# Optimization experiments

Measured on AMD Instinct MI355X. Metric: run time of the kernel, lower is better.

The kernel has to match this reference:

```python
import jax, jax.numpy as jnp
import numpy as np

CPV = 64  # cpv_size; output_size = CPV*(CPV+1)//2 = 2080

def _tri_indices(cpv):
    # Reproduce the torch nested-loop scatter order:
    # for idx_x in range(cpv): for idx_y in range(cpv-idx_x): col = cpv-1-idx_y
    rows = np.repeat(np.arange(cpv), cpv - np.arange(cpv))
    cols = np.concatenate([np.arange(cpv - 1, i - 1, -1) for i in range(cpv)])
    return jnp.asarray(rows), jnp.asarray(cols)


def setup_inputs() -> dict:
    key = jax.random.key(0)
    ks = jax.random.split(key, 12)
    B, D_in, H, L = 8192, 1024, 2048, CPV * (CPV + 1) // 2
    s = lambda fan_in: 1.0 / np.sqrt(fan_in)
    return {
        "x":   jax.random.normal(ks[0], (B, D_in), jnp.float32),
        "W1":  jax.random.uniform(ks[1], (D_in, H), jnp.float32, -s(D_in), s(D_in)),
        "b1":  jnp.zeros((H,), jnp.float32),
        "W2":  jax.random.uniform(ks[2], (H, H), jnp.float32, -s(H), s(H)),
        "b2":  jnp.zeros((H,), jnp.float32),
        "W21": jax.random.uniform(ks[3], (H, H), jnp.float32, -s(H), s(H)),
        "b21": jnp.zeros((H,), jnp.float32),
        "W22": jax.random.uniform(ks[4], (H, H), jnp.float32, -s(H), s(H)),
        "b22": jnp.zeros((H,), jnp.float32),
        "W3":  jax.random.uniform(ks[5], (H, L), jnp.float32, -s(H), s(H)),
        "b3":  jnp.zeros((L,), jnp.float32),
    }


def reference(x, W1, b1, W2, b2, W21, b21, W22, b22, W3, b3):
    lrelu = lambda t: jax.nn.leaky_relu(t, 0.01)
    h = lrelu(x @ W1 + b1)
    h = lrelu(h @ W2 + b2)
    h = lrelu(h @ W21 + b21)
    h = lrelu(h @ W22 + b22)
    y = h @ W3 + b3  # [B, L] with L = CPV*(CPV+1)//2
    rows, cols = _tri_indices(CPV)
    is_diag = rows == cols  # diagonal entries are abs'ed (negated when <= 0)
    vals = jnp.where(is_diag[None, :] & (y <= 0), -y, y)
    B = y.shape[0]
    M = jnp.zeros((B, CPV, CPV), y.dtype).at[:, rows, cols].set(vals)
    return jnp.transpose(M, (1, 2, 0))  # torch stacks per-example matrices on dim=2
```

## Files before the change

kernel.cpp:

```cpp
#include <hip/hip_runtime.h>
#include <hip/hip_bf16.h>
#include <stdint.h>

typedef short short8 __attribute__((ext_vector_type(8)));
typedef float f32x4  __attribute__((ext_vector_type(4)));

typedef __attribute__((address_space(1))) uint32_t u32_g;
typedef __attribute__((address_space(3))) uint32_t u32_l;

#define BM 128
#define BN 128
#define BK 64

__device__ __forceinline__ void gld_lds16(const void* g, const void* l) {
  __builtin_amdgcn_global_load_lds((u32_g*)(uintptr_t)g, (u32_l*)(uintptr_t)l, 16, 0, 0);
}

template <int FINAL>
__global__ __launch_bounds__(256) void gemm_k(
    const __hip_bfloat16* __restrict__ A,
    const __hip_bfloat16* __restrict__ BT,
    const float* __restrict__ bias,
    __hip_bfloat16* __restrict__ Cb,
    float* __restrict__ Cf,
    const int* __restrict__ tbl,
    int K, int Nreal)
{
  __shared__ __attribute__((aligned(16))) __hip_bfloat16 As[BM * BK];
  __shared__ __attribute__((aligned(16))) __hip_bfloat16 Bs[BN * BK];

  const int tid  = threadIdx.x;
  const int lane = tid & 63;
  const int l15  = lane & 15;
  const int quad = lane >> 4;
  const int wave = tid >> 6;
  const int wm   = (wave >> 1) << 6;
  const int wn   = (wave & 1) << 6;

  const int bm = blockIdx.x * BM;
  const int bn = blockIdx.y * BN;

  const __hip_bfloat16* ag[4];
  const __hip_bfloat16* bg[4];
  uint32_t lofs[4];
#pragma unroll
  for (int c = 0; c < 4; ++c) {
    int ci   = tid + 256 * c;
    int row  = ci >> 3;
    int chk  = ci & 7;
    int gchk = chk ^ (row & 7);
    ag[c]   = A  + (size_t)(bm + row) * K + gchk * 8;
    bg[c]   = BT + (size_t)(bn + row) * K + gchk * 8;
    lofs[c] = (uint32_t)ci * 16u;
  }

  f32x4 acc[4][4];
#pragma unroll
  for (int i = 0; i < 4; ++i)
#pragma unroll
    for (int j = 0; j < 4; ++j)
      acc[i][j] = (f32x4){0.f, 0.f, 0.f, 0.f};

  const int nk = K >> 6;
  for (int kt = 0; kt < nk; ++kt) {
#pragma unroll
    for (int c = 0; c < 4; ++c) {
      gld_lds16(ag[c], (const char*)As + lofs[c]);
      gld_lds16(bg[c], (const char*)Bs + lofs[c]);
      ag[c] += BK;
      bg[c] += BK;
    }
    __syncthreads();
#pragma unroll
    for (int ks = 0; ks < 2; ++ks) {
      short8 af[4], bf[4];
      const int cf = ks * 4 + quad;
#pragma unroll
      for (int i = 0; i < 4; ++i) {
        int m  = wm + i * 16 + l15;
        int sc = cf ^ (m & 7);
        af[i]  = *(const short8*)(As + m * BK + sc * 8);
      }
#pragma unroll
      for (int j = 0; j < 4; ++j) {
        int n  = wn + j * 16 + l15;
        int sc = cf ^ (n & 7);
        bf[j]  = *(const short8*)(Bs + n * BK + sc * 8);
      }
#pragma unroll
      for (int i = 0; i < 4; ++i)
#pragma unroll
        for (int j = 0; j < 4; ++j)
          acc[i][j] = __builtin_amdgcn_mfma_f32_16x16x32_bf16(af[i], bf[j], acc[i][j], 0, 0, 0);
    }
    __syncthreads();
  }

  if (FINAL == 0) {
#pragma unroll
    for (int j = 0; j < 4; ++j) {
      int   n  = bn + wn + j * 16 + l15;
      float bv = bias[n];
#pragma unroll
      for (int i = 0; i < 4; ++i) {
        int m0 = bm + wm + i * 16 + quad * 4;
#pragma unroll
        for (int r = 0; r < 4; ++r) {
          float v = acc[i][j][r] + bv;
          v = (v > 0.f) ? v : 0.01f * v;
          Cb[(size_t)(m0 + r) * 2048 + n] = __float2bfloat16(v);
        }
      }
    }
  } else {
#pragma unroll
    for (int j = 0; j < 4; ++j) {
      int n = bn + wn + j * 16 + l15;
      if (n < Nreal) {
        float bv   = bias[n];
        int  code  = tbl[n];
        int  dst   = code & 4095;
        bool diag  = (code & 4096) != 0;
#pragma unroll
        for (int i = 0; i < 4; ++i) {
          int m0 = bm + wm + i * 16 + quad * 4;
          f32x4 pk;
#pragma unroll
          for (int r = 0; r < 4; ++r) {
            float v = acc[i][j][r] + bv;
            if (diag) v = fabsf(v);
            pk[r] = v;
          }
          *reinterpret_cast<f32x4*>(Cf + (size_t)dst * 8192 + m0) = pk;
        }
      }
    }
  }
}

__global__ void transpose_k(const float* __restrict__ in,
                            __hip_bfloat16* __restrict__ out,
                            int K, int N)
{
  __shared__ __hip_bfloat16 t[32][33];
  const int n0 = blockIdx.x * 32;
  const int k0 = blockIdx.y * 32;
  const int tx = threadIdx.x, ty = threadIdx.y;
  const __hip_bfloat16 zero = __float2bfloat16(0.f);
#pragma unroll
  for (int r = 0; r < 32; r += 8) {
    int k = k0 + ty + r, n = n0 + tx;
    t[ty + r][tx] = (n < N) ? __float2bfloat16(in[(size_t)k * N + n]) : zero;
  }
  __syncthreads();
#pragma unroll
  for (int r = 0; r < 32; r += 8) {
    int n = n0 + ty + r;
    out[(size_t)n * K + k0 + tx] = t[tx][ty + r];
  }
}

__global__ void cvt_k(const float* __restrict__ in,
                      __hip_bfloat16* __restrict__ out, int n)
{
  int i = (blockIdx.x * 256 + threadIdx.x) * 4;
  if (i >= n) return;
  float4 v = *reinterpret_cast<const float4*>(in + i);
  union { unsigned short us[4]; uint2 v2; } pk;
  __hip_bfloat16 h;
  h = __float2bfloat16(v.x); pk.us[0] = *reinterpret_cast<unsigned short*>(&h);
  h = __float2bfloat16(v.y); pk.us[1] = *reinterpret_cast<unsigned short*>(&h);
  h = __float2bfloat16(v.z); pk.us[2] = *reinterpret_cast<unsigned short*>(&h);
  h = __float2bfloat16(v.w); pk.us[3] = *reinterpret_cast<unsigned short*>(&h);
  *reinterpret_cast<uint2*>(out + i) = pk.v2;
}

__global__ void table_k(int* __restrict__ tbl)
{
  int l = blockIdx.x * 64 + threadIdx.x;
  if (l >= 2080) return;
  int r = 0, s = 0;
  while (s + (64 - r) <= l) { s += 64 - r; ++r; }
  int c = 63 - (l - s);
  tbl[l] = (r * 64 + c) | ((r == c) ? 4096 : 0);
}

extern "C" void kernel_launch(void* const* d_in, const int* in_sizes, int n_in,
                              void* d_out, int out_size, void* d_ws, size_t ws_size,
                              hipStream_t stream)
{
  const float* x   = (const float*)d_in[0];
  const float* W1  = (const float*)d_in[1];
  const float* b1  = (const float*)d_in[2];
  const float* W2  = (const float*)d_in[3];
  const float* b2  = (const float*)d_in[4];
  const float* W21 = (const float*)d_in[5];
  const float* b21 = (const float*)d_in[6];
  const float* W22 = (const float*)d_in[7];
  const float* b22 = (const float*)d_in[8];
  const float* W3  = (const float*)d_in[9];
  const float* b3  = (const float*)d_in[10];
  float* out = (float*)d_out;

  char* ws = (char*)d_ws;
  __hip_bfloat16* act0 = (__hip_bfloat16*)(ws);
  __hip_bfloat16* act1 = (__hip_bfloat16*)(ws + ((size_t)32 << 20));
  __hip_bfloat16* xb   = act1;
  __hip_bfloat16* W1T  = (__hip_bfloat16*)(ws + ((size_t)64 << 20));
  __hip_bfloat16* W2T  = (__hip_bfloat16*)(ws + ((size_t)68 << 20));
  __hip_bfloat16* W21T = (__hip_bfloat16*)(ws + ((size_t)76 << 20));
  __hip_bfloat16* W22T = (__hip_bfloat16*)(ws + ((size_t)84 << 20));
  __hip_bfloat16* W3T  = (__hip_bfloat16*)(ws + ((size_t)92 << 20));
  int*            tbl  = (int*)(ws + ((size_t)101 << 20));

  hipMemsetAsync(d_out, 0, (size_t)out_size * sizeof(float), stream);
  table_k<<<33, 64, 0, stream>>>(tbl);

  cvt_k<<<8192, 256, 0, stream>>>(x, xb, 8192 * 1024);

  dim3 tb(32, 8);
  transpose_k<<<dim3(64, 32), tb, 0, stream>>>(W1,  W1T,  1024, 2048);
  transpose_k<<<dim3(64, 64), tb, 0, stream>>>(W2,  W2T,  2048, 2048);
  transpose_k<<<dim3(64, 64), tb, 0, stream>>>(W21, W21T, 2048, 2048);
  transpose_k<<<dim3(64, 64), tb, 0, stream>>>(W22, W22T, 2048, 2048);
  transpose_k<<<dim3(68, 64), tb, 0, stream>>>(W3,  W3T,  2048, 2080);

  gemm_k<0><<<dim3(64, 16), 256, 0, stream>>>(xb,   W1T,  b1,  act0, nullptr, nullptr, 1024, 2048);
  gemm_k<0><<<dim3(64, 16), 256, 0, stream>>>(act0, W2T,  b2,  act1, nullptr, nullptr, 2048, 2048);
  gemm_k<0><<<dim3(64, 16), 256, 0, stream>>>(act1, W21T, b21, act0, nullptr, nullptr, 2048, 2048);
  gemm_k<0><<<dim3(64, 16), 256, 0, stream>>>(act0, W22T, b22, act1, nullptr, nullptr, 2048, 2048);
  gemm_k<1><<<dim3(64, 17), 256, 0, stream>>>(act1, W3T,  b3,  nullptr, out,  tbl,     2048, 2080);
}
```

Before: 615.3 us.

## Use 256x256 tiles with triple-buffered async LDS pipeline and fused zero fill

```diff
diff --git a/kernel.cpp b/kernel.cpp
--- a/kernel.cpp
+++ b/kernel.cpp
@@ -8,16 +8,18 @@
 typedef __attribute__((address_space(1))) uint32_t u32_g;
 typedef __attribute__((address_space(3))) uint32_t u32_l;
 
-#define BM 128
-#define BN 128
-#define BK 64
+#define BM 256
+#define BN 256
+#define BK 32
+#define SLOTB 32768
+#define BOFF  16384
 
 __device__ __forceinline__ void gld_lds16(const void* g, const void* l) {
   __builtin_amdgcn_global_load_lds((u32_g*)(uintptr_t)g, (u32_l*)(uintptr_t)l, 16, 0, 0);
 }
 
 template <int FINAL>
-__global__ __launch_bounds__(256) void gemm_k(
+__global__ __launch_bounds__(512, 2) void gemm_k(
     const __hip_bfloat16* __restrict__ A,
     const __hip_bfloat16* __restrict__ BT,
     const float* __restrict__ bias,
@@ -26,74 +28,105 @@
     const int* __restrict__ tbl,
     int K, int Nreal)
 {
-  __shared__ __attribute__((aligned(16))) __hip_bfloat16 As[BM * BK];
-  __shared__ __attribute__((aligned(16))) __hip_bfloat16 Bs[BN * BK];
+  __shared__ __attribute__((aligned(16))) char smem[3 * SLOTB];
 
   const int tid  = threadIdx.x;
   const int lane = tid & 63;
   const int l15  = lane & 15;
   const int quad = lane >> 4;
   const int wave = tid >> 6;
-  const int wm   = (wave >> 1) << 6;
-  const int wn   = (wave & 1) << 6;
+  const int wm   = (wave >> 2) * 128;
+  const int wn   = (wave & 3) * 64;
 
   const int bm = blockIdx.x * BM;
   const int bn = blockIdx.y * BN;
 
-  const __hip_bfloat16* ag[4];
-  const __hip_bfloat16* bg[4];
-  uint32_t lofs[4];
-#pragma unroll
-  for (int c = 0; c < 4; ++c) {
-    int ci   = tid + 256 * c;
-    int row  = ci >> 3;
-    int chk  = ci & 7;
-    int gchk = chk ^ (row & 7);
-    ag[c]   = A  + (size_t)(bm + row) * K + gchk * 8;
-    bg[c]   = BT + (size_t)(bn + row) * K + gchk * 8;
-    lofs[c] = (uint32_t)ci * 16u;
-  }
-
-  f32x4 acc[4][4];
-#pragma unroll
-  for (int i = 0; i < 4; ++i)
+  const int arow = wm + l15;
+  const uint32_t aoff = (uint32_t)arow * 64u + (uint32_t)(((quad + (arow >> 1)) & 3) << 4);
+  const int brow = wn + l15;
+  const uint32_t boff = BOFF + (uint32_t)brow * 64u + (uint32_t)(((quad + (brow >> 1)) & 3) << 4);
+
+  const __hip_bfloat16* ag[2];
+  const __hip_bfloat16* bg[2];
+  uint32_t dA[2], dB[2];
+#pragma unroll
+  for (int c = 0; c < 2; ++c) {
+    int ci  = tid + 512 * c;
+    int row = ci >> 2;
+    int gc  = ((ci & 3) - (row >> 1)) & 3;
+    ag[c] = A  + (size_t)(bm + row) * K + gc * 8;
+    bg[c] = BT + (size_t)(bn + row) * K + gc * 8;
+    dA[c] = (uint32_t)ci * 16u;
+    dB[c] = BOFF + (uint32_t)ci * 16u;
+  }
+
+  f32x4 acc[8][4];
+#pragma unroll
+  for (int i = 0; i < 8; ++i)
 #pragma unroll
     for (int j = 0; j < 4; ++j)
       acc[i][j] = (f32x4){0.f, 0.f, 0.f, 0.f};
 
-  const int nk = K >> 6;
-  for (int kt = 0; kt < nk; ++kt) {
-#pragma unroll
-    for (int c = 0; c < 4; ++c) {
-      gld_lds16(ag[c], (const char*)As + lofs[c]);
-      gld_lds16(bg[c], (const char*)Bs + lofs[c]);
+  const int nk = K >> 5;
+
+#pragma unroll
+  for (int t = 0; t < 2; ++t) {
+    char* stb = smem + t * SLOTB;
+#pragma unroll
+    for (int c = 0; c < 2; ++c) {
+      gld_lds16(ag[c], stb + dA[c]);
+      gld_lds16(bg[c], stb + dB[c]);
       ag[c] += BK;
       bg[c] += BK;
     }
-    __syncthreads();
-#pragma unroll
-    for (int ks = 0; ks < 2; ++ks) {
-      short8 af[4], bf[4];
-      const int cf = ks * 4 + quad;
-#pragma unroll
-      for (int i = 0; i < 4; ++i) {
-        int m  = wm + i * 16 + l15;
-        int sc = cf ^ (m & 7);
-        af[i]  = *(const short8*)(As + m * BK + sc * 8);
+  }
+
+  int cur = 0, nst = 2;
+  for (int kt = 0; kt < nk; ++kt) {
+    if (kt < nk - 1) asm volatile("s_waitcnt vmcnt(4) lgkmcnt(0)" ::: "memory");
+    else             asm volatile("s_waitcnt vmcnt(0) lgkmcnt(0)" ::: "memory");
+    __builtin_amdgcn_s_barrier();
+    asm volatile("" ::: "memory");
+
+    const char* rb  = smem + cur * SLOTB;
+    char*       stb = smem + nst * SLOTB;
+
+    if (kt < nk - 2) {
+#pragma unroll
+      for (int c = 0; c < 2; ++c) {
+        gld_lds16(ag[c], stb + dA[c]);
+        gld_lds16(bg[c], stb + dB[c]);
+        ag[c] += BK;
+        bg[c] += BK;
       }
-#pragma unroll
-      for (int j = 0; j < 4; ++j) {
-        int n  = wn + j * 16 + l15;
-        int sc = cf ^ (n & 7);
-        bf[j]  = *(const short8*)(Bs + n * BK + sc * 8);
-      }
-#pragma unroll
-      for (int i = 0; i < 4; ++i)
-#pragma unroll
-        for (int j = 0; j < 4; ++j)
-          acc[i][j] = __builtin_amdgcn_mfma_f32_16x16x32_bf16(af[i], bf[j], acc[i][j], 0, 0, 0);
-    }
-    __syncthreads();
+    }
+
+    short8 bf[4], af[4];
+#pragma unroll
+    for (int j = 0; j < 4; ++j) bf[j] = *(const short8*)(rb + boff + j * 1024);
+#pragma unroll
+    for (int i = 0; i < 4; ++i) af[i] = *(const short8*)(rb + aoff + i * 1024);
+    __builtin_amdgcn_s_setprio(1);
+#pragma unroll
+    for (int i = 0; i < 4; ++i)
+#pragma unroll
+      for (int j = 0; j < 4; ++j)
+        acc[i][j] = __builtin_amdgcn_mfma_f32_16x16x32_bf16(af[i], bf[j], acc[i][j], 0, 0, 0);
+    __builtin_amdgcn_s_setprio(0);
+
+    short8 af2[4];
+#pragma unroll
+    for (int i = 0; i < 4; ++i) af2[i] = *(const short8*)(rb + aoff + 4096 + i * 1024);
+    __builtin_amdgcn_s_setprio(1);
+#pragma unroll
+    for (int i = 0; i < 4; ++i)
+#pragma unroll
+      for (int j = 0; j < 4; ++j)
+        acc[i + 4][j] = __builtin_amdgcn_mfma_f32_16x16x32_bf16(af2[i], bf[j], acc[i + 4][j], 0, 0, 0);
+    __builtin_amdgcn_s_setprio(0);
+
+    cur = (cur == 2) ? 0 : cur + 1;
+    nst = (nst == 2) ? 0 : nst + 1;
   }
 
   if (FINAL == 0) {
@@ -102,7 +135,7 @@
       int   n  = bn + wn + j * 16 + l15;
       float bv = bias[n];
 #pragma unroll
-      for (int i = 0; i < 4; ++i) {
+      for (int i = 0; i < 8; ++i) {
         int m0 = bm + wm + i * 16 + quad * 4;
 #pragma unroll
         for (int r = 0; r < 4; ++r) {
@@ -121,8 +154,10 @@
         int  code  = tbl[n];
         int  dst   = code & 4095;
         bool diag  = (code & 4096) != 0;
-#pragma unroll
-        for (int i = 0; i < 4; ++i) {
+        int  mir   = ((dst & 63) << 6) | (dst >> 6);
+        const f32x4 z = (f32x4){0.f, 0.f, 0.f, 0.f};
+#pragma unroll
+        for (int i = 0; i < 8; ++i) {
           int m0 = bm + wm + i * 16 + quad * 4;
           f32x4 pk;
 #pragma unroll
@@ -132,6 +167,8 @@
             pk[r] = v;
           }
           *reinterpret_cast<f32x4*>(Cf + (size_t)dst * 8192 + m0) = pk;
+          if (!diag)
+            *reinterpret_cast<f32x4*>(Cf + (size_t)mir * 8192 + m0) = z;
         }
       }
     }
@@ -213,7 +250,6 @@
   __hip_bfloat16* W3T  = (__hip_bfloat16*)(ws + ((size_t)92 << 20));
   int*            tbl  = (int*)(ws + ((size_t)101 << 20));
 
-  hipMemsetAsync(d_out, 0, (size_t)out_size * sizeof(float), stream);
   table_k<<<33, 64, 0, stream>>>(tbl);
 
   cvt_k<<<8192, 256, 0, stream>>>(x, xb, 8192 * 1024);
@@ -223,11 +259,11 @@
   transpose_k<<<dim3(64, 64), tb, 0, stream>>>(W2,  W2T,  2048, 2048);
   transpose_k<<<dim3(64, 64), tb, 0, stream>>>(W21, W21T, 2048, 2048);
   transpose_k<<<dim3(64, 64), tb, 0, stream>>>(W22, W22T, 2048, 2048);
-  transpose_k<<<dim3(68, 64), tb, 0, stream>>>(W3,  W3T,  2048, 2080);
-
-  gemm_k<0><<<dim3(64, 16), 256, 0, stream>>>(xb,   W1T,  b1,  act0, nullptr, nullptr, 1024, 2048);
-  gemm_k<0><<<dim3(64, 16), 256, 0, stream>>>(act0, W2T,  b2,  act1, nullptr, nullptr, 2048, 2048);
-  gemm_k<0><<<dim3(64, 16), 256, 0, stream>>>(act1, W21T, b21, act0, nullptr, nullptr, 2048, 2048);
-  gemm_k<0><<<dim3(64, 16), 256, 0, stream>>>(act0, W22T, b22, act1, nullptr, nullptr, 2048, 2048);
-  gemm_k<1><<<dim3(64, 17), 256, 0, stream>>>(act1, W3T,  b3,  nullptr, out,  tbl,     2048, 2080);
-}
+  transpose_k<<<dim3(72, 64), tb, 0, stream>>>(W3,  W3T,  2048, 2080);
+
+  gemm_k<0><<<dim3(32, 8), 512, 0, stream>>>(xb,   W1T,  b1,  act0, nullptr, nullptr, 1024, 2048);
+  gemm_k<0><<<dim3(32, 8), 512, 0, stream>>>(act0, W2T,  b2,  act1, nullptr, nullptr, 2048, 2048);
+  gemm_k<0><<<dim3(32, 8), 512, 0, stream>>>(act1, W21T, b21, act0, nullptr, nullptr, 2048, 2048);
+  gemm_k<0><<<dim3(32, 8), 512, 0, stream>>>(act0, W22T, b22, act1, nullptr, nullptr, 2048, 2048);
+  gemm_k<1><<<dim3(32, 9), 512, 0, stream>>>(act1, W3T,  b3,  nullptr, out,  tbl,     2048, 2080);
+}
```

New measurement: 607.3 us. About the same (-1.3%).

## Coalesce bf16 epilogue via LDS and replace output memset with mirrored zero stores

Applied to the files above, without the earlier changes.

```diff
diff --git a/kernel.cpp b/kernel.cpp
--- a/kernel.cpp
+++ b/kernel.cpp
@@ -26,8 +26,7 @@
     const int* __restrict__ tbl,
     int K, int Nreal)
 {
-  __shared__ __attribute__((aligned(16))) __hip_bfloat16 As[BM * BK];
-  __shared__ __attribute__((aligned(16))) __hip_bfloat16 Bs[BN * BK];
+  __shared__ __attribute__((aligned(16))) char smem[33792];
 
   const int tid  = threadIdx.x;
   const int lane = tid & 63;
@@ -65,8 +64,8 @@
   for (int kt = 0; kt < nk; ++kt) {
 #pragma unroll
     for (int c = 0; c < 4; ++c) {
-      gld_lds16(ag[c], (const char*)As + lofs[c]);
-      gld_lds16(bg[c], (const char*)Bs + lofs[c]);
+      gld_lds16(ag[c], smem + lofs[c]);
+      gld_lds16(bg[c], smem + 16384 + lofs[c]);
       ag[c] += BK;
       bg[c] += BK;
     }
@@ -79,13 +78,13 @@
       for (int i = 0; i < 4; ++i) {
         int m  = wm + i * 16 + l15;
         int sc = cf ^ (m & 7);
-        af[i]  = *(const short8*)(As + m * BK + sc * 8);
+        af[i]  = *(const short8*)(smem + m * 128 + sc * 16);
       }
 #pragma unroll
       for (int j = 0; j < 4; ++j) {
         int n  = wn + j * 16 + l15;
         int sc = cf ^ (n & 7);
-        bf[j]  = *(const short8*)(Bs + n * BK + sc * 8);
+        bf[j]  = *(const short8*)(smem + 16384 + n * 128 + sc * 16);
       }
 #pragma unroll
       for (int i = 0; i < 4; ++i)
@@ -99,18 +98,27 @@
   if (FINAL == 0) {
 #pragma unroll
     for (int j = 0; j < 4; ++j) {
-      int   n  = bn + wn + j * 16 + l15;
-      float bv = bias[n];
+      int   n  = wn + j * 16 + l15;
+      float bv = bias[bn + n];
 #pragma unroll
       for (int i = 0; i < 4; ++i) {
-        int m0 = bm + wm + i * 16 + quad * 4;
+        int m0 = wm + i * 16 + quad * 4;
 #pragma unroll
         for (int r = 0; r < 4; ++r) {
           float v = acc[i][j][r] + bv;
           v = (v > 0.f) ? v : 0.01f * v;
-          Cb[(size_t)(m0 + r) * 2048 + n] = __float2bfloat16(v);
+          *(__hip_bfloat16*)(smem + (m0 + r) * 264 + n * 2) = __float2bfloat16(v);
         }
       }
+    }
+    __syncthreads();
+    const int rr = tid >> 4;
+    const int cb = (tid & 15) * 16;
+#pragma unroll
+    for (int p = 0; p < 8; ++p) {
+      int row = p * 16 + rr;
+      short8 v = *(const short8*)(smem + row * 264 + cb);
+      *reinterpret_cast<short8*>((char*)Cb + ((size_t)(bm + row) * 2048 + bn) * 2 + cb) = v;
     }
   } else {
 #pragma unroll
@@ -121,6 +129,8 @@
         int  code  = tbl[n];
         int  dst   = code & 4095;
         bool diag  = (code & 4096) != 0;
+        int  mir   = ((dst & 63) << 6) | (dst >> 6);
+        const f32x4 z = (f32x4){0.f, 0.f, 0.f, 0.f};
 #pragma unroll
         for (int i = 0; i < 4; ++i) {
           int m0 = bm + wm + i * 16 + quad * 4;
@@ -132,6 +142,8 @@
             pk[r] = v;
           }
           *reinterpret_cast<f32x4*>(Cf + (size_t)dst * 8192 + m0) = pk;
+          if (!diag)
+            *reinterpret_cast<f32x4*>(Cf + (size_t)mir * 8192 + m0) = z;
         }
       }
     }
@@ -213,7 +225,6 @@
   __hip_bfloat16* W3T  = (__hip_bfloat16*)(ws + ((size_t)92 << 20));
   int*            tbl  = (int*)(ws + ((size_t)101 << 20));
 
-  hipMemsetAsync(d_out, 0, (size_t)out_size * sizeof(float), stream);
   table_k<<<33, 64, 0, stream>>>(tbl);
 
   cvt_k<<<8192, 256, 0, stream>>>(x, xb, 8192 * 1024);
```

New measurement: 635.4 us. 1.03x slower.
